# Kernel tuning notes

Hardware: AMD Instinct MI355X
Metric: run time of the kernel (lower is better)

The kernel has to match this reference:

```python
import jax, jax.numpy as jnp
import numpy as np

BLOCK_SIZE = 64

def quantize_dequantize(w, block_size=BLOCK_SIZE):
    # LPBQ double quantization: block-wise abs-max -> uint4 scale1 over fp32 scale2
    out_ch, in_ch = w.shape
    pad_len = (block_size - in_ch % block_size) % block_size
    if pad_len > 0:
        w = jnp.pad(w, ((0, 0), (0, pad_len)))
    wr = w.reshape(out_ch, -1, block_size)                      # [O, nB, B]
    s1 = jnp.clip(jnp.max(jnp.abs(wr), axis=-1, keepdims=True) / 7.0, 1e-8)   # [O, nB, 1]
    s2 = jnp.clip(jnp.max(s1, axis=1, keepdims=True) / 15.0, 1e-8)            # [O, 1, 1]
    s1_q = jnp.clip(jnp.round(s1 / s2), 0.0, 15.0)
    s1_recon = s1_q * s2
    w_q = jnp.clip(jnp.round(wr / s1_recon), -8.0, 7.0)
    w_recon = (w_q * s1_recon).reshape(out_ch, -1)
    if pad_len > 0:
        w_recon = w_recon[:, :-pad_len]
    return w_recon

def setup_inputs() -> dict:
    key = jax.random.key(0)
    k1, k2, k3 = jax.random.split(key, 3)
    B, S, IN, OUT = 1, 128, 4096, 11008
    x = jax.random.normal(k1, (B, S, IN), dtype=jnp.float32)
    weight = jax.random.normal(k2, (OUT, IN), dtype=jnp.float32)
    bias = jax.random.normal(k3, (OUT,), dtype=jnp.float32)
    return {"x": x, "weight": weight, "bias": bias}

def reference(x, weight, bias):
    w_q = quantize_dequantize(weight)
    # F.linear: x @ w_q.T + bias
    return jnp.einsum('bsi,oi->bso', x, w_q) + bias
```

## Files before the change

### kernel.cpp

```cpp
#include <hip/hip_runtime.h>
#include <hip/hip_bf16.h>

#define IN_CH 4096
#define OUT_CH 11008
#define QBLK 64

#define BM 128
#define BN 64
#define BK 64
#define KCHUNKS (IN_CH / BK)
#define KSPLIT 4
#define SPLIT_CHUNKS (KCHUNKS / KSPLIT)
#define NTILES (OUT_CH / BN)
#define XCONV_BLOCKS 16
#define BPAD 72

typedef short bf16x8 __attribute__((ext_vector_type(8)));
typedef float f32x4 __attribute__((ext_vector_type(4)));
typedef char char16v __attribute__((ext_vector_type(16)));

#define GLOBAL_AS __attribute__((address_space(1)))
#define LDS_AS __attribute__((address_space(3)))

__device__ inline unsigned short f2bf(float f) {
    union { __hip_bfloat16 h; unsigned short u; } cv;
    cv.h = __float2bfloat16(f);
    return cv.u;
}

__global__ __launch_bounds__(256) void quant_kernel(
        const float* __restrict__ w, const float* __restrict__ x,
        signed char* __restrict__ wq, float* __restrict__ s1rT,
        unsigned short* __restrict__ xq) {
    const int tid = threadIdx.x;

    if (blockIdx.x >= OUT_CH) {
        const int bx = blockIdx.x - OUT_CH;
        for (int it = 0; it < 16; ++it) {
            const int G = it * 4096 + bx * 256 + tid;
            const int row = G >> 9;
            const int gi = G & 511;
            const int kc = gi >> 3;
            const int gp = gi & 7;
            const int gl = gp ^ (row & 7);
            const float4* src =
                (const float4*)(x + (size_t)row * IN_CH + kc * 64 + gl * 8);
            float4 a = src[0], b = src[1];
            ushort4 o0, o1;
            o0.x = f2bf(a.x); o0.y = f2bf(a.y); o0.z = f2bf(a.z); o0.w = f2bf(a.w);
            o1.x = f2bf(b.x); o1.y = f2bf(b.y); o1.z = f2bf(b.z); o1.w = f2bf(b.w);
            ushort4* dst = (ushort4*)(xq + (size_t)row * IN_CH + gi * 8);
            dst[0] = o0;
            dst[1] = o1;
        }
        return;
    }

    const int row = blockIdx.x;
    const float* wrow = w + (size_t)row * IN_CH;
    signed char* orow = wq + (size_t)row * IN_CH;

    __shared__ float s1_lds[64];

    float4 v[4];
    const int lane16 = tid & 15;

    for (int p = 0; p < 4; ++p) {
        v[p] = ((const float4*)wrow)[p * 256 + tid];
        float m = fmaxf(fmaxf(fabsf(v[p].x), fabsf(v[p].y)),
                        fmaxf(fabsf(v[p].z), fabsf(v[p].w)));
        m = fmaxf(m, __shfl_xor(m, 1));
        m = fmaxf(m, __shfl_xor(m, 2));
        m = fmaxf(m, __shfl_xor(m, 4));
        m = fmaxf(m, __shfl_xor(m, 8));
        if (lane16 == 0)
            s1_lds[p * 16 + (tid >> 4)] = fmaxf(m * (1.0f / 7.0f), 1e-8f);
    }
    __syncthreads();

    if (tid < 64) {
        float s1 = s1_lds[tid];
        float m = s1;
        m = fmaxf(m, __shfl_xor(m, 1));
        m = fmaxf(m, __shfl_xor(m, 2));
        m = fmaxf(m, __shfl_xor(m, 4));
        m = fmaxf(m, __shfl_xor(m, 8));
        m = fmaxf(m, __shfl_xor(m, 16));
        m = fmaxf(m, __shfl_xor(m, 32));
        const float s2 = fmaxf(m * (1.0f / 15.0f), 1e-8f);
        const float s1q = fminf(fmaxf(rintf(s1 / s2), 0.0f), 15.0f);
        const float s1r = s1q * s2;
        s1_lds[tid] = s1r;
        s1rT[(size_t)tid * OUT_CH + row] = s1r;
    }
    __syncthreads();

    for (int p = 0; p < 4; ++p) {
        const float s1r = s1_lds[p * 16 + (tid >> 4)];
        char4 o;
        o.x = (signed char)(int)fminf(fmaxf(rintf(v[p].x / s1r), -8.0f), 7.0f);
        o.y = (signed char)(int)fminf(fmaxf(rintf(v[p].y / s1r), -8.0f), 7.0f);
        o.z = (signed char)(int)fminf(fmaxf(rintf(v[p].z / s1r), -8.0f), 7.0f);
        o.w = (signed char)(int)fminf(fmaxf(rintf(v[p].w / s1r), -8.0f), 7.0f);
        ((char4*)orow)[p * 256 + tid] = o;
    }
}

__global__ __launch_bounds__(256) void gemm_kernel(
        const unsigned short* __restrict__ A, const signed char* __restrict__ WQ,
        const float* __restrict__ s1rT, float* __restrict__ part) {
    __shared__ __align__(16) unsigned short ldsA[BM * BK];
    __shared__ __align__(16) unsigned short ldsB[BN * BPAD];

    const int tid = threadIdx.x;
    const int w = tid >> 6;
    const int l = tid & 63;
    const int wm = w >> 1;
    const int wn = w & 1;
    const int n0 = blockIdx.x * BN;
    const int kc0 = blockIdx.y * SPLIT_CHUNKS;

    const int r8 = l >> 3;
    const int sg = l & 7;

    const int brow = tid >> 2;
    const int bcg = tid & 3;

    f32x4 acc[4][2] = {};

    const int lane15 = l & 15;
    const int quad = l >> 4;

    for (int kc = kc0; kc < kc0 + SPLIT_CHUNKS; ++kc) {
        const int k0 = kc * BK;

        for (int i = 0; i < 4; ++i) {
            const unsigned short* gp =
                A + (size_t)(i * 32 + w * 8 + r8) * IN_CH + k0 + sg * 8;
            LDS_AS unsigned short* lp =
                (LDS_AS unsigned short*)&ldsA[(i * 32 + w * 8) * BK];
            __builtin_amdgcn_global_load_lds((const GLOBAL_AS void*)gp,
                                             (LDS_AS void*)lp, 16, 0, 0);
        }

        const float s1 = s1rT[(size_t)kc * OUT_CH + n0 + brow];
        char16v bq = *(const char16v*)(WQ + (size_t)(n0 + brow) * IN_CH +
                                       k0 + bcg * 16);
        bf16x8 o0, o1;
        for (int i = 0; i < 8; ++i)
            o0[i] = (short)f2bf((float)bq[i] * s1);
        for (int i = 0; i < 8; ++i)
            o1[i] = (short)f2bf((float)bq[8 + i] * s1);
        *(bf16x8*)&ldsB[brow * BPAD + bcg * 16] = o0;
        *(bf16x8*)&ldsB[brow * BPAD + bcg * 16 + 8] = o1;

        asm volatile("s_waitcnt vmcnt(0)" ::: "memory");
        __syncthreads();

        for (int kk = 0; kk < 2; ++kk) {
            bf16x8 af[4], bfv[2];
            const int ko = kk * 32 + quad * 8;
            for (int i = 0; i < 4; ++i) {
                const int row = wm * 64 + i * 16 + lane15;
                const int pg = ((kk * 4 + quad) ^ (row & 7)) * 8;
                af[i] = *(const bf16x8*)&ldsA[row * BK + pg];
            }
            for (int j = 0; j < 2; ++j)
                bfv[j] = *(const bf16x8*)&ldsB[(wn * 32 + j * 16 + lane15) * BPAD + ko];
            for (int i = 0; i < 4; ++i)
                for (int j = 0; j < 2; ++j)
                    acc[i][j] = __builtin_amdgcn_mfma_f32_16x16x32_bf16(
                        af[i], bfv[j], acc[i][j], 0, 0, 0);
        }
        __syncthreads();
    }

    float* pbase = part + (size_t)blockIdx.y * BM * OUT_CH;
    const int m_base = wm * 64 + quad * 4;
    const int n_base = n0 + wn * 32 + lane15;
    for (int j = 0; j < 2; ++j) {
        for (int i = 0; i < 4; ++i) {
            const int m = m_base + i * 16;
            float* cp = pbase + (size_t)m * OUT_CH + n_base + j * 16;
            cp[0 * OUT_CH] = acc[i][j][0];
            cp[1 * OUT_CH] = acc[i][j][1];
            cp[2 * OUT_CH] = acc[i][j][2];
            cp[3 * OUT_CH] = acc[i][j][3];
        }
    }
}

__global__ __launch_bounds__(256) void reduce_kernel(
        const float* __restrict__ part, const float* __restrict__ bias,
        float* __restrict__ out) {
    const int m = blockIdx.y;
    const int x4 = blockIdx.x * 256 + threadIdx.x;
    if (x4 >= OUT_CH / 4) return;
    const size_t off = (size_t)m * OUT_CH + x4 * 4;

    float4 acc = ((const float4*)bias)[x4];
    for (int s = 0; s < KSPLIT; ++s) {
        float4 p = *(const float4*)(part + (size_t)s * BM * OUT_CH + off);
        acc.x += p.x; acc.y += p.y; acc.z += p.z; acc.w += p.w;
    }
    *(float4*)(out + off) = acc;
}

extern "C" void kernel_launch(void* const* d_in, const int* in_sizes, int n_in,
                              void* d_out, int out_size, void* d_ws, size_t ws_size,
                              hipStream_t stream) {
    const float* x = (const float*)d_in[0];
    const float* weight = (const float*)d_in[1];
    const float* bias = (const float*)d_in[2];
    float* out = (float*)d_out;

    signed char* wsQ = (signed char*)d_ws;
    unsigned short* wsX = (unsigned short*)(wsQ + (size_t)OUT_CH * IN_CH);
    float* wsS = (float*)(wsX + (size_t)BM * IN_CH);
    float* wsP = wsS + (size_t)QBLK * OUT_CH;

    quant_kernel<<<OUT_CH + XCONV_BLOCKS, 256, 0, stream>>>(weight, x, wsQ, wsS, wsX);
    gemm_kernel<<<dim3(NTILES, KSPLIT), 256, 0, stream>>>(wsX, wsQ, wsS, wsP);
    reduce_kernel<<<dim3((OUT_CH / 4 + 255) / 256, BM), 256, 0, stream>>>(
        wsP, bias, out);
}
```

Baseline: 291.9 us.

## Pack quantized weights to int4 and double-buffer GEMM LDS tiles

The quant kernel now packs two int4 weight values per byte, halving the intermediate weight buffer written and then read back by the GEMM. The GEMM gains double-buffered LDS for the A and B tiles, so the next chunk's global loads are issued before the current chunk's MFMAs and the nibbles are unpacked into the other buffer afterwards. This targets memory traffic and load latency, at the cost of twice the LDS, extra nibble-unpacking ALU work, and more registers held across the MFMA loop.

```diff
diff --git a/kernel.cpp b/kernel.cpp
--- a/kernel.cpp
+++ b/kernel.cpp
@@ -17,7 +17,6 @@
 
 typedef short bf16x8 __attribute__((ext_vector_type(8)));
 typedef float f32x4 __attribute__((ext_vector_type(4)));
-typedef char char16v __attribute__((ext_vector_type(16)));
 
 #define GLOBAL_AS __attribute__((address_space(1)))
 #define LDS_AS __attribute__((address_space(3)))
@@ -26,6 +25,17 @@
     union { __hip_bfloat16 h; unsigned short u; } cv;
     cv.h = __float2bfloat16(f);
     return cv.u;
+}
+
+__device__ inline void unpack8(unsigned v, float s1, bf16x8& o) {
+#pragma unroll
+    for (int i = 0; i < 4; ++i) {
+        const int byte = (int)((v >> (8 * i)) & 0xFF);
+        const int lo = (byte << 28) >> 28;
+        const int hi = (byte << 24) >> 28;
+        o[2 * i]     = (short)f2bf((float)lo * s1);
+        o[2 * i + 1] = (short)f2bf((float)hi * s1);
+    }
 }
 
 __global__ __launch_bounds__(256) void quant_kernel(
@@ -58,7 +68,7 @@
 
     const int row = blockIdx.x;
     const float* wrow = w + (size_t)row * IN_CH;
-    signed char* orow = wq + (size_t)row * IN_CH;
+    signed char* orow = wq + (size_t)row * (IN_CH / 2);
 
     __shared__ float s1_lds[64];
 
@@ -97,20 +107,22 @@
 
     for (int p = 0; p < 4; ++p) {
         const float s1r = s1_lds[p * 16 + (tid >> 4)];
-        char4 o;
-        o.x = (signed char)(int)fminf(fmaxf(rintf(v[p].x / s1r), -8.0f), 7.0f);
-        o.y = (signed char)(int)fminf(fmaxf(rintf(v[p].y / s1r), -8.0f), 7.0f);
-        o.z = (signed char)(int)fminf(fmaxf(rintf(v[p].z / s1r), -8.0f), 7.0f);
-        o.w = (signed char)(int)fminf(fmaxf(rintf(v[p].w / s1r), -8.0f), 7.0f);
-        ((char4*)orow)[p * 256 + tid] = o;
+        const int q0 = (int)fminf(fmaxf(rintf(v[p].x / s1r), -8.0f), 7.0f);
+        const int q1 = (int)fminf(fmaxf(rintf(v[p].y / s1r), -8.0f), 7.0f);
+        const int q2 = (int)fminf(fmaxf(rintf(v[p].z / s1r), -8.0f), 7.0f);
+        const int q3 = (int)fminf(fmaxf(rintf(v[p].w / s1r), -8.0f), 7.0f);
+        char2 o;
+        o.x = (signed char)((q0 & 0xF) | ((q1 & 0xF) << 4));
+        o.y = (signed char)((q2 & 0xF) | ((q3 & 0xF) << 4));
+        ((char2*)orow)[p * 256 + tid] = o;
     }
 }
 
 __global__ __launch_bounds__(256) void gemm_kernel(
-        const unsigned short* __restrict__ A, const signed char* __restrict__ WQ,
+        const unsigned short* __restrict__ A, const signed char* __restrict__ WQ4,
         const float* __restrict__ s1rT, float* __restrict__ part) {
-    __shared__ __align__(16) unsigned short ldsA[BM * BK];
-    __shared__ __align__(16) unsigned short ldsB[BN * BPAD];
+    __shared__ __align__(16) unsigned short ldsA[2][BM * BK];
+    __shared__ __align__(16) unsigned short ldsB[2][BN * BPAD];
 
     const int tid = threadIdx.x;
     const int w = tid >> 6;
@@ -126,36 +138,55 @@
     const int brow = tid >> 2;
     const int bcg = tid & 3;
 
-    f32x4 acc[4][2] = {};
-
     const int lane15 = l & 15;
     const int quad = l >> 4;
 
-    for (int kc = kc0; kc < kc0 + SPLIT_CHUNKS; ++kc) {
-        const int k0 = kc * BK;
-
+    f32x4 acc[4][2] = {};
+
+    const size_t bqBase = (size_t)(n0 + brow) * (IN_CH / 2) + bcg * 8;
+
+    {
+        const int k0 = kc0 * BK;
         for (int i = 0; i < 4; ++i) {
             const unsigned short* gp =
                 A + (size_t)(i * 32 + w * 8 + r8) * IN_CH + k0 + sg * 8;
             LDS_AS unsigned short* lp =
-                (LDS_AS unsigned short*)&ldsA[(i * 32 + w * 8) * BK];
+                (LDS_AS unsigned short*)&ldsA[0][(i * 32 + w * 8) * BK];
             __builtin_amdgcn_global_load_lds((const GLOBAL_AS void*)gp,
                                              (LDS_AS void*)lp, 16, 0, 0);
         }
-
-        const float s1 = s1rT[(size_t)kc * OUT_CH + n0 + brow];
-        char16v bq = *(const char16v*)(WQ + (size_t)(n0 + brow) * IN_CH +
-                                       k0 + bcg * 16);
+        const float s1 = s1rT[(size_t)kc0 * OUT_CH + n0 + brow];
+        const uint2 bq = *(const uint2*)(WQ4 + bqBase + (size_t)kc0 * 32);
         bf16x8 o0, o1;
-        for (int i = 0; i < 8; ++i)
-            o0[i] = (short)f2bf((float)bq[i] * s1);
-        for (int i = 0; i < 8; ++i)
-            o1[i] = (short)f2bf((float)bq[8 + i] * s1);
-        *(bf16x8*)&ldsB[brow * BPAD + bcg * 16] = o0;
-        *(bf16x8*)&ldsB[brow * BPAD + bcg * 16 + 8] = o1;
-
+        unpack8(bq.x, s1, o0);
+        unpack8(bq.y, s1, o1);
+        *(bf16x8*)&ldsB[0][brow * BPAD + bcg * 16] = o0;
+        *(bf16x8*)&ldsB[0][brow * BPAD + bcg * 16 + 8] = o1;
         asm volatile("s_waitcnt vmcnt(0)" ::: "memory");
         __syncthreads();
+    }
+
+    for (int t = 0; t < SPLIT_CHUNKS; ++t) {
+        const int cur = t & 1;
+        const int nxt = cur ^ 1;
+        const bool has_next = (t + 1 < SPLIT_CHUNKS);
+
+        uint2 bqn;
+        float s1n;
+        if (has_next) {
+            const int kcn = kc0 + t + 1;
+            const int k0n = kcn * BK;
+            for (int i = 0; i < 4; ++i) {
+                const unsigned short* gp =
+                    A + (size_t)(i * 32 + w * 8 + r8) * IN_CH + k0n + sg * 8;
+                LDS_AS unsigned short* lp =
+                    (LDS_AS unsigned short*)&ldsA[nxt][(i * 32 + w * 8) * BK];
+                __builtin_amdgcn_global_load_lds((const GLOBAL_AS void*)gp,
+                                                 (LDS_AS void*)lp, 16, 0, 0);
+            }
+            s1n = s1rT[(size_t)kcn * OUT_CH + n0 + brow];
+            bqn = *(const uint2*)(WQ4 + bqBase + (size_t)kcn * 32);
+        }
 
         for (int kk = 0; kk < 2; ++kk) {
             bf16x8 af[4], bfv[2];
@@ -163,14 +194,23 @@
             for (int i = 0; i < 4; ++i) {
                 const int row = wm * 64 + i * 16 + lane15;
                 const int pg = ((kk * 4 + quad) ^ (row & 7)) * 8;
-                af[i] = *(const bf16x8*)&ldsA[row * BK + pg];
+                af[i] = *(const bf16x8*)&ldsA[cur][row * BK + pg];
             }
             for (int j = 0; j < 2; ++j)
-                bfv[j] = *(const bf16x8*)&ldsB[(wn * 32 + j * 16 + lane15) * BPAD + ko];
+                bfv[j] = *(const bf16x8*)&ldsB[cur][(wn * 32 + j * 16 + lane15) * BPAD + ko];
             for (int i = 0; i < 4; ++i)
                 for (int j = 0; j < 2; ++j)
                     acc[i][j] = __builtin_amdgcn_mfma_f32_16x16x32_bf16(
                         af[i], bfv[j], acc[i][j], 0, 0, 0);
+        }
+
+        if (has_next) {
+            bf16x8 o0, o1;
+            unpack8(bqn.x, s1n, o0);
+            unpack8(bqn.y, s1n, o1);
+            *(bf16x8*)&ldsB[nxt][brow * BPAD + bcg * 16] = o0;
+            *(bf16x8*)&ldsB[nxt][brow * BPAD + bcg * 16 + 8] = o1;
+            asm volatile("s_waitcnt vmcnt(0)" ::: "memory");
         }
         __syncthreads();
     }
@@ -215,7 +255,7 @@
     float* out = (float*)d_out;
 
     signed char* wsQ = (signed char*)d_ws;
-    unsigned short* wsX = (unsigned short*)(wsQ + (size_t)OUT_CH * IN_CH);
+    unsigned short* wsX = (unsigned short*)(wsQ + (size_t)OUT_CH * (IN_CH / 2));
     float* wsS = (float*)(wsX + (size_t)BM * IN_CH);
     float* wsP = wsS + (size_t)QBLK * OUT_CH;
 
```

New measurement: 293.8 us. No clear change (+0.6%).

## Fuse weight quantize-dequantize into GEMM and drop split-K reduction

Applied to the files above, without the earlier changes.

Replaces the separate weight-quantization, split-K GEMM and reduction kernels with a single fused kernel. Each block computes block scales for its 32 output rows, then streams the fp32 weights again, quantize-dequantizes them into bf16 in LDS and runs MFMA with double-buffered A/B tiles, adding bias in the epilogue. This removes the int8 weight and scale round trips through global memory, the partial-sum buffers and the reduction launch, in exchange for reading the fp32 weights twice and using fewer, larger-LDS blocks with no K split.

```diff
diff --git a/kernel.cpp b/kernel.cpp
--- a/kernel.cpp
+++ b/kernel.cpp
@@ -3,21 +3,17 @@
 
 #define IN_CH 4096
 #define OUT_CH 11008
-#define QBLK 64
 
 #define BM 128
-#define BN 64
+#define BN 32
 #define BK 64
 #define KCHUNKS (IN_CH / BK)
-#define KSPLIT 4
-#define SPLIT_CHUNKS (KCHUNKS / KSPLIT)
-#define NTILES (OUT_CH / BN)
-#define XCONV_BLOCKS 16
+#define NBLOCKS (OUT_CH / BN)
 #define BPAD 72
+#define XCONV_BLOCKS 64
 
 typedef short bf16x8 __attribute__((ext_vector_type(8)));
 typedef float f32x4 __attribute__((ext_vector_type(4)));
-typedef char char16v __attribute__((ext_vector_type(16)));
 
 #define GLOBAL_AS __attribute__((address_space(1)))
 #define LDS_AS __attribute__((address_space(3)))
@@ -28,182 +24,176 @@
     return cv.u;
 }
 
-__global__ __launch_bounds__(256) void quant_kernel(
-        const float* __restrict__ w, const float* __restrict__ x,
-        signed char* __restrict__ wq, float* __restrict__ s1rT,
-        unsigned short* __restrict__ xq) {
+__device__ inline bf16x8 qdq8(float4 a, float4 b, float s) {
+    bf16x8 o;
+    const float v0 = a.x, v1 = a.y, v2 = a.z, v3 = a.w;
+    const float v4 = b.x, v5 = b.y, v6 = b.z, v7 = b.w;
+    o[0] = (short)f2bf(fminf(fmaxf(rintf(v0 / s), -8.0f), 7.0f) * s);
+    o[1] = (short)f2bf(fminf(fmaxf(rintf(v1 / s), -8.0f), 7.0f) * s);
+    o[2] = (short)f2bf(fminf(fmaxf(rintf(v2 / s), -8.0f), 7.0f) * s);
+    o[3] = (short)f2bf(fminf(fmaxf(rintf(v3 / s), -8.0f), 7.0f) * s);
+    o[4] = (short)f2bf(fminf(fmaxf(rintf(v4 / s), -8.0f), 7.0f) * s);
+    o[5] = (short)f2bf(fminf(fmaxf(rintf(v5 / s), -8.0f), 7.0f) * s);
+    o[6] = (short)f2bf(fminf(fmaxf(rintf(v6 / s), -8.0f), 7.0f) * s);
+    o[7] = (short)f2bf(fminf(fmaxf(rintf(v7 / s), -8.0f), 7.0f) * s);
+    return o;
+}
+
+__global__ __launch_bounds__(256) void xconv_kernel(
+        const float* __restrict__ x, unsigned short* __restrict__ xq) {
     const int tid = threadIdx.x;
-
-    if (blockIdx.x >= OUT_CH) {
-        const int bx = blockIdx.x - OUT_CH;
-        for (int it = 0; it < 16; ++it) {
-            const int G = it * 4096 + bx * 256 + tid;
-            const int row = G >> 9;
-            const int gi = G & 511;
-            const int kc = gi >> 3;
-            const int gp = gi & 7;
-            const int gl = gp ^ (row & 7);
-            const float4* src =
-                (const float4*)(x + (size_t)row * IN_CH + kc * 64 + gl * 8);
-            float4 a = src[0], b = src[1];
-            ushort4 o0, o1;
-            o0.x = f2bf(a.x); o0.y = f2bf(a.y); o0.z = f2bf(a.z); o0.w = f2bf(a.w);
-            o1.x = f2bf(b.x); o1.y = f2bf(b.y); o1.z = f2bf(b.z); o1.w = f2bf(b.w);
-            ushort4* dst = (ushort4*)(xq + (size_t)row * IN_CH + gi * 8);
-            dst[0] = o0;
-            dst[1] = o1;
-        }
-        return;
-    }
-
-    const int row = blockIdx.x;
-    const float* wrow = w + (size_t)row * IN_CH;
-    signed char* orow = wq + (size_t)row * IN_CH;
-
-    __shared__ float s1_lds[64];
-
-    float4 v[4];
-    const int lane16 = tid & 15;
-
-    for (int p = 0; p < 4; ++p) {
-        v[p] = ((const float4*)wrow)[p * 256 + tid];
-        float m = fmaxf(fmaxf(fabsf(v[p].x), fabsf(v[p].y)),
-                        fmaxf(fabsf(v[p].z), fabsf(v[p].w)));
+    const int bx = blockIdx.x;
+    for (int it = 0; it < 4; ++it) {
+        const int G = it * (XCONV_BLOCKS * 256) + bx * 256 + tid;
+        const int row = G >> 9;
+        const int gi = G & 511;
+        const int kc = gi >> 3;
+        const int gp = gi & 7;
+        const int gl = gp ^ (row & 7);
+        const float4* src =
+            (const float4*)(x + (size_t)row * IN_CH + kc * 64 + gl * 8);
+        float4 a = src[0], b = src[1];
+        ushort4 o0, o1;
+        o0.x = f2bf(a.x); o0.y = f2bf(a.y); o0.z = f2bf(a.z); o0.w = f2bf(a.w);
+        o1.x = f2bf(b.x); o1.y = f2bf(b.y); o1.z = f2bf(b.z); o1.w = f2bf(b.w);
+        ushort4* dst = (ushort4*)(xq + (size_t)row * IN_CH + gi * 8);
+        dst[0] = o0;
+        dst[1] = o1;
+    }
+}
+
+__global__ __launch_bounds__(256) void fused_kernel(
+        const float* __restrict__ w, const unsigned short* __restrict__ A,
+        const float* __restrict__ bias, float* __restrict__ out) {
+    __shared__ float s1_lds[BN][KCHUNKS];
+    __shared__ __align__(16) unsigned short ldsA[2][BM * BK];
+    __shared__ __align__(16) unsigned short ldsB[2][BN * BPAD];
+
+    const int tid = threadIdx.x;
+    const int n0 = blockIdx.x * BN;
+
+    const int prow = tid >> 3;
+    const int pc8 = (tid & 7) * 8;
+
+    const float* wrow = w + (size_t)(n0 + prow) * IN_CH + pc8;
+#pragma unroll 4
+    for (int c = 0; c < KCHUNKS; ++c) {
+        float4 a = *(const float4*)(wrow + c * 64);
+        float4 b = *(const float4*)(wrow + c * 64 + 4);
+        float m = fmaxf(fmaxf(fabsf(a.x), fabsf(a.y)),
+                        fmaxf(fabsf(a.z), fabsf(a.w)));
+        m = fmaxf(m, fmaxf(fmaxf(fabsf(b.x), fabsf(b.y)),
+                           fmaxf(fabsf(b.z), fabsf(b.w))));
         m = fmaxf(m, __shfl_xor(m, 1));
         m = fmaxf(m, __shfl_xor(m, 2));
         m = fmaxf(m, __shfl_xor(m, 4));
-        m = fmaxf(m, __shfl_xor(m, 8));
-        if (lane16 == 0)
-            s1_lds[p * 16 + (tid >> 4)] = fmaxf(m * (1.0f / 7.0f), 1e-8f);
+        if ((tid & 7) == 0)
+            s1_lds[prow][c] = fmaxf(m * (1.0f / 7.0f), 1e-8f);
     }
     __syncthreads();
 
-    if (tid < 64) {
-        float s1 = s1_lds[tid];
-        float m = s1;
+    {
+        float sv[8];
+        float m = 0.0f;
+#pragma unroll
+        for (int k = 0; k < 8; ++k) {
+            sv[k] = s1_lds[prow][pc8 + k];
+            m = fmaxf(m, sv[k]);
+        }
         m = fmaxf(m, __shfl_xor(m, 1));
         m = fmaxf(m, __shfl_xor(m, 2));
         m = fmaxf(m, __shfl_xor(m, 4));
-        m = fmaxf(m, __shfl_xor(m, 8));
-        m = fmaxf(m, __shfl_xor(m, 16));
-        m = fmaxf(m, __shfl_xor(m, 32));
         const float s2 = fmaxf(m * (1.0f / 15.0f), 1e-8f);
-        const float s1q = fminf(fmaxf(rintf(s1 / s2), 0.0f), 15.0f);
-        const float s1r = s1q * s2;
-        s1_lds[tid] = s1r;
-        s1rT[(size_t)tid * OUT_CH + row] = s1r;
+#pragma unroll
+        for (int k = 0; k < 8; ++k) {
+            const float s1q = fminf(fmaxf(rintf(sv[k] / s2), 0.0f), 15.0f);
+            s1_lds[prow][pc8 + k] = s1q * s2;
+        }
     }
     __syncthreads();
 
-    for (int p = 0; p < 4; ++p) {
-        const float s1r = s1_lds[p * 16 + (tid >> 4)];
-        char4 o;
-        o.x = (signed char)(int)fminf(fmaxf(rintf(v[p].x / s1r), -8.0f), 7.0f);
-        o.y = (signed char)(int)fminf(fmaxf(rintf(v[p].y / s1r), -8.0f), 7.0f);
-        o.z = (signed char)(int)fminf(fmaxf(rintf(v[p].z / s1r), -8.0f), 7.0f);
-        o.w = (signed char)(int)fminf(fmaxf(rintf(v[p].w / s1r), -8.0f), 7.0f);
-        ((char4*)orow)[p * 256 + tid] = o;
-    }
-}
-
-__global__ __launch_bounds__(256) void gemm_kernel(
-        const unsigned short* __restrict__ A, const signed char* __restrict__ WQ,
-        const float* __restrict__ s1rT, float* __restrict__ part) {
-    __shared__ __align__(16) unsigned short ldsA[BM * BK];
-    __shared__ __align__(16) unsigned short ldsB[BN * BPAD];
-
-    const int tid = threadIdx.x;
-    const int w = tid >> 6;
+    const int wid = tid >> 6;
     const int l = tid & 63;
-    const int wm = w >> 1;
-    const int wn = w & 1;
-    const int n0 = blockIdx.x * BN;
-    const int kc0 = blockIdx.y * SPLIT_CHUNKS;
-
+    const int wm = wid >> 1;
+    const int wn = wid & 1;
     const int r8 = l >> 3;
     const int sg = l & 7;
-
-    const int brow = tid >> 2;
-    const int bcg = tid & 3;
-
-    f32x4 acc[4][2] = {};
-
     const int lane15 = l & 15;
     const int quad = l >> 4;
 
-    for (int kc = kc0; kc < kc0 + SPLIT_CHUNKS; ++kc) {
-        const int k0 = kc * BK;
-
+    const float* wB = w + (size_t)(n0 + prow) * IN_CH + pc8;
+
+    f32x4 acc[4] = {};
+
+    {
+        float4 b0 = *(const float4*)(wB);
+        float4 b1 = *(const float4*)(wB + 4);
         for (int i = 0; i < 4; ++i) {
             const unsigned short* gp =
-                A + (size_t)(i * 32 + w * 8 + r8) * IN_CH + k0 + sg * 8;
+                A + (size_t)(i * 32 + wid * 8 + r8) * IN_CH + sg * 8;
             LDS_AS unsigned short* lp =
-                (LDS_AS unsigned short*)&ldsA[(i * 32 + w * 8) * BK];
+                (LDS_AS unsigned short*)&ldsA[0][(i * 32 + wid * 8) * BK];
             __builtin_amdgcn_global_load_lds((const GLOBAL_AS void*)gp,
                                              (LDS_AS void*)lp, 16, 0, 0);
         }
-
-        const float s1 = s1rT[(size_t)kc * OUT_CH + n0 + brow];
-        char16v bq = *(const char16v*)(WQ + (size_t)(n0 + brow) * IN_CH +
-                                       k0 + bcg * 16);
-        bf16x8 o0, o1;
-        for (int i = 0; i < 8; ++i)
-            o0[i] = (short)f2bf((float)bq[i] * s1);
-        for (int i = 0; i < 8; ++i)
-            o1[i] = (short)f2bf((float)bq[8 + i] * s1);
-        *(bf16x8*)&ldsB[brow * BPAD + bcg * 16] = o0;
-        *(bf16x8*)&ldsB[brow * BPAD + bcg * 16 + 8] = o1;
-
+        const float s = s1_lds[prow][0];
+        *(bf16x8*)&ldsB[0][prow * BPAD + pc8] = qdq8(b0, b1, s);
         asm volatile("s_waitcnt vmcnt(0)" ::: "memory");
         __syncthreads();
+    }
+
+    for (int t = 0; t < KCHUNKS; ++t) {
+        const int cur = t & 1;
+        const int nxt = cur ^ 1;
+        const bool has_next = (t + 1 < KCHUNKS);
+
+        float4 b0, b1;
+        if (has_next) {
+            const int k0n = (t + 1) * BK;
+            b0 = *(const float4*)(wB + k0n);
+            b1 = *(const float4*)(wB + k0n + 4);
+            for (int i = 0; i < 4; ++i) {
+                const unsigned short* gp =
+                    A + (size_t)(i * 32 + wid * 8 + r8) * IN_CH + k0n + sg * 8;
+                LDS_AS unsigned short* lp =
+                    (LDS_AS unsigned short*)&ldsA[nxt][(i * 32 + wid * 8) * BK];
+                __builtin_amdgcn_global_load_lds((const GLOBAL_AS void*)gp,
+                                                 (LDS_AS void*)lp, 16, 0, 0);
+            }
+        }
 
         for (int kk = 0; kk < 2; ++kk) {
-            bf16x8 af[4], bfv[2];
+            bf16x8 af[4], bfv;
             const int ko = kk * 32 + quad * 8;
             for (int i = 0; i < 4; ++i) {
                 const int row = wm * 64 + i * 16 + lane15;
                 const int pg = ((kk * 4 + quad) ^ (row & 7)) * 8;
-                af[i] = *(const bf16x8*)&ldsA[row * BK + pg];
+                af[i] = *(const bf16x8*)&ldsA[cur][row * BK + pg];
             }
-            for (int j = 0; j < 2; ++j)
-                bfv[j] = *(const bf16x8*)&ldsB[(wn * 32 + j * 16 + lane15) * BPAD + ko];
+            bfv = *(const bf16x8*)&ldsB[cur][(wn * 16 + lane15) * BPAD + ko];
             for (int i = 0; i < 4; ++i)
-                for (int j = 0; j < 2; ++j)
-                    acc[i][j] = __builtin_amdgcn_mfma_f32_16x16x32_bf16(
-                        af[i], bfv[j], acc[i][j], 0, 0, 0);
+                acc[i] = __builtin_amdgcn_mfma_f32_16x16x32_bf16(
+                    af[i], bfv, acc[i], 0, 0, 0);
+        }
+
+        if (has_next) {
+            const float s = s1_lds[prow][t + 1];
+            *(bf16x8*)&ldsB[nxt][prow * BPAD + pc8] = qdq8(b0, b1, s);
+            asm volatile("s_waitcnt vmcnt(0)" ::: "memory");
         }
         __syncthreads();
     }
 
-    float* pbase = part + (size_t)blockIdx.y * BM * OUT_CH;
     const int m_base = wm * 64 + quad * 4;
-    const int n_base = n0 + wn * 32 + lane15;
-    for (int j = 0; j < 2; ++j) {
-        for (int i = 0; i < 4; ++i) {
-            const int m = m_base + i * 16;
-            float* cp = pbase + (size_t)m * OUT_CH + n_base + j * 16;
-            cp[0 * OUT_CH] = acc[i][j][0];
-            cp[1 * OUT_CH] = acc[i][j][1];
-            cp[2 * OUT_CH] = acc[i][j][2];
-            cp[3 * OUT_CH] = acc[i][j][3];
-        }
-    }
-}
-
-__global__ __launch_bounds__(256) void reduce_kernel(
-        const float* __restrict__ part, const float* __restrict__ bias,
-        float* __restrict__ out) {
-    const int m = blockIdx.y;
-    const int x4 = blockIdx.x * 256 + threadIdx.x;
-    if (x4 >= OUT_CH / 4) return;
-    const size_t off = (size_t)m * OUT_CH + x4 * 4;
-
-    float4 acc = ((const float4*)bias)[x4];
-    for (int s = 0; s < KSPLIT; ++s) {
-        float4 p = *(const float4*)(part + (size_t)s * BM * OUT_CH + off);
-        acc.x += p.x; acc.y += p.y; acc.z += p.z; acc.w += p.w;
-    }
-    *(float4*)(out + off) = acc;
+    const int nn = n0 + wn * 16 + lane15;
+    const float bv = bias[nn];
+    for (int i = 0; i < 4; ++i) {
+        float* cp = out + (size_t)(m_base + i * 16) * OUT_CH + nn;
+        cp[0 * OUT_CH] = acc[i][0] + bv;
+        cp[1 * OUT_CH] = acc[i][1] + bv;
+        cp[2 * OUT_CH] = acc[i][2] + bv;
+        cp[3 * OUT_CH] = acc[i][3] + bv;
+    }
 }
 
 extern "C" void kernel_launch(void* const* d_in, const int* in_sizes, int n_in,
@@ -214,13 +204,8 @@
     const float* bias = (const float*)d_in[2];
     float* out = (float*)d_out;
 
-    signed char* wsQ = (signed char*)d_ws;
-    unsigned short* wsX = (unsigned short*)(wsQ + (size_t)OUT_CH * IN_CH);
-    float* wsS = (float*)(wsX + (size_t)BM * IN_CH);
-    float* wsP = wsS + (size_t)QBLK * OUT_CH;
-
-    quant_kernel<<<OUT_CH + XCONV_BLOCKS, 256, 0, stream>>>(weight, x, wsQ, wsS, wsX);
-    gemm_kernel<<<dim3(NTILES, KSPLIT), 256, 0, stream>>>(wsX, wsQ, wsS, wsP);
-    reduce_kernel<<<dim3((OUT_CH / 4 + 255) / 256, BM), 256, 0, stream>>>(
-        wsP, bias, out);
-}
+    unsigned short* wsX = (unsigned short*)d_ws;
+
+    xconv_kernel<<<XCONV_BLOCKS, 256, 0, stream>>>(x, wsX);
+    fused_kernel<<<NBLOCKS, 256, 0, stream>>>(weight, wsX, bias, out);
+}
```

After: 330.6 us. 13.2% more time.
